# Kernel optimization log

Hardware: AMD Instinct MI355X
Metric: run time of the kernel (lower is better)

The kernel has to match this reference:

```python
import jax, jax.numpy as jnp
import numpy as np
import math

N_HEAD = 8
N_EMBD = 128  # per-head dim and input feature dim
WIN_LEN = 2048
SUB_LEN = 64
Q_LEN = 5
BATCH = 2
NEG = -1e9


def _row_mask(index, sub_len, win_len):
    log_l = math.ceil(np.log2(sub_len))
    mask = np.zeros(win_len, dtype=np.float32)
    if (win_len // sub_len) * 2 * log_l > index:
        mask[: index + 1] = 1
    else:
        while index >= 0:
            if index - log_l + 1 < 0:
                mask[:index] = 1
                break
            mask[index - log_l + 1 : index + 1] = 1  # local attention
            for i in range(log_l):
                new_index = index - log_l + 1 - 2 ** i
                if (index - new_index) <= sub_len and new_index >= 0:
                    mask[new_index] = 1  # restart attention
            index -= sub_len
    return mask


def log_mask(win_len, sub_len):
    m = np.stack([_row_mask(i, sub_len, win_len) for i in range(win_len)], axis=0)
    return m.reshape(1, 1, win_len, win_len)


def entmax15(X):
    # 1.5-entmax along the last axis, full sort (k=None path of the torch code)
    X = (X - jnp.max(X, axis=-1, keepdims=True)) * 0.5
    Xsrt = -jnp.sort(-X, axis=-1)  # descending
    d = X.shape[-1]
    rho = jnp.arange(1, d + 1, dtype=X.dtype)
    mean = jnp.cumsum(Xsrt, axis=-1) / rho
    mean_sq = jnp.cumsum(Xsrt * Xsrt, axis=-1) / rho
    ss = rho * (mean_sq - mean * mean)
    delta = (1.0 - ss) / rho
    tau = mean - jnp.sqrt(jnp.clip(delta, 0.0))
    support_size = jnp.sum(tau <= Xsrt, axis=-1, keepdims=True)
    tau_star = jnp.take_along_axis(tau, support_size - 1, axis=-1)
    Y = jnp.clip(X - tau_star, 0.0)
    return Y * Y


def setup_inputs() -> dict:
    key = jax.random.key(0)
    ks = jax.random.split(key, 5)
    H, D = N_HEAD, N_EMBD
    x = jax.random.normal(ks[0], (BATCH, WIN_LEN, D), dtype=jnp.float32)
    mask = jnp.asarray(log_mask(WIN_LEN, SUB_LEN))
    std = 0.02
    w_qk = jax.random.normal(ks[1], (2 * H * D, D, Q_LEN), dtype=jnp.float32) * std
    b_qk = jnp.zeros((2 * H * D,), jnp.float32)
    w_v = jax.random.normal(ks[2], (D, H * D), dtype=jnp.float32) * std
    b_v = jnp.zeros((H * D,), jnp.float32)
    w_proj = jax.random.normal(ks[3], (H * D, D), dtype=jnp.float32) * std
    b_proj = jnp.zeros((D,), jnp.float32)
    return {"x": x, "mask": mask, "w_qk": w_qk, "b_qk": b_qk,
            "w_v": w_v, "b_v": b_v, "w_proj": w_proj, "b_proj": b_proj}


def reference(x, mask, w_qk, b_qk, w_v, b_v, w_proj, b_proj):
    B, S, D = x.shape
    H = N_HEAD
    # value projection (Conv1D rf=1 == linear)
    value = x @ w_v + b_v                              # [B,S,H*D]
    # causal conv for query/key: left-pad by q_len-1
    xc = jnp.transpose(x, (0, 2, 1))                   # [B,D,S]
    qk = jax.lax.conv_general_dilated(
        xc, w_qk, window_strides=(1,), padding=[(Q_LEN - 1, 0)],
        dimension_numbers=("NCH", "OIH", "NCH"))       # [B,2HD,S]
    qk = jnp.transpose(qk, (0, 2, 1)) + b_qk           # [B,S,2HD]
    query, key = jnp.split(qk, 2, axis=-1)
    q = query.reshape(B, S, H, D).transpose(0, 2, 1, 3)   # [B,H,S,D]
    k = key.reshape(B, S, H, D).transpose(0, 2, 1, 3)     # [B,H,S,D]
    v = value.reshape(B, S, H, D).transpose(0, 2, 1, 3)   # [B,H,S,D]
    pre = jnp.einsum("bhqd,bhkd->bhqk", q, k)            # [B,H,S,S]
    pre = pre / jnp.sqrt(jnp.asarray(D, pre.dtype))      # scale=True
    m = mask[:, :, :S, :S]
    pre = pre * m + NEG * (1.0 - m)
    att = entmax15(pre)                                  # sparse normalizer
    # dropout is identity in eval mode
    out = jnp.einsum("bhqk,bhkd->bhqd", att, v)          # [B,H,S,D]
    out = out.transpose(0, 2, 1, 3).reshape(B, S, H * D)  # merge heads
    out = out @ w_proj + b_proj                           # c_proj
    return out
```

## Files before the change

### kernel.cpp

```cpp
#include <hip/hip_runtime.h>
#include <hip/hip_bf16.h>
#include <hip/hip_fp16.h>

#define S_LEN 2048
#define BATCH 2
#define DIM 128
#define NH 8
#define HD 1024
#define QL 5
#define KKTOT 640
#define OCH 2048
#define MAXNNZ 384

typedef _Float16 hv2 __attribute__((ext_vector_type(2)));
typedef _Float16 f16x8 __attribute__((ext_vector_type(8)));
typedef float f32x4 __attribute__((ext_vector_type(4)));

#if defined(__has_builtin)
#  if __has_builtin(__builtin_amdgcn_fdot2)
#    define USE_FDOT2 1
#  endif
#endif
#ifndef USE_FDOT2
#  define USE_FDOT2 0
#endif

__device__ __forceinline__ hv2 u2h(unsigned u) {
    union { unsigned u; hv2 h; } c; c.u = u; return c.h;
}
__device__ __forceinline__ float dot2acc(unsigned a, unsigned b, float acc) {
#if USE_FDOT2
    return __builtin_amdgcn_fdot2(u2h(a), u2h(b), acc, false);
#else
    hv2 ha = u2h(a), hb = u2h(b);
    return acc + (float)ha[0] * (float)hb[0] + (float)ha[1] * (float)hb[1];
#endif
}

__global__ void k_cvt_x(const float4* __restrict__ src, ushort4* __restrict__ dst, int n4) {
    int i = blockIdx.x * 256 + threadIdx.x;
    if (i >= n4) return;
    float4 v = src[i];
    ushort4 o;
    o.x = __half_as_ushort(__float2half(v.x));
    o.y = __half_as_ushort(__float2half(v.y));
    o.z = __half_as_ushort(__float2half(v.z));
    o.w = __half_as_ushort(__float2half(v.w));
    dst[i] = o;
}

__global__ void k_wqk_t(const float* __restrict__ w, _Float16* __restrict__ bt) {
    int j = blockIdx.x * 256 + threadIdx.x;
    if (j >= OCH * KKTOT) return;
    int o = j / KKTOT;
    int k = j % KKTOT;
    int t = k >> 7, i = k & 127;
    bt[j] = (_Float16)w[(size_t)o * KKTOT + i * QL + t];
}

__global__ void k_wv_t(const float* __restrict__ wv, _Float16* __restrict__ wvt) {
    int j = blockIdx.x * 256 + threadIdx.x;
    if (j >= HD * DIM) return;
    int c = j >> 7, k = j & 127;
    wvt[j] = (_Float16)wv[(size_t)k * HD + c];
}

__global__ void k_wp_t(const float* __restrict__ wp, _Float16* __restrict__ wpt) {
    int j = blockIdx.x * 256 + threadIdx.x;
    if (j >= DIM * HD) return;
    int c = j >> 10, k = j & 1023;
    wpt[j] = (_Float16)wp[(size_t)k * DIM + c];
}

__global__ void k_mask_csr(const float* __restrict__ mask, unsigned* __restrict__ cnt,
                           unsigned* __restrict__ idx) {
    __shared__ unsigned s_base;
    __shared__ unsigned s_wcnt[4];
    int r = blockIdx.x;
    int tid = threadIdx.x;
    int lane = tid & 63;
    int w = tid >> 6;
    if (tid == 0) s_base = 0;
    __syncthreads();
    for (int c0 = 0; c0 < S_LEN; c0 += 256) {
        int c = c0 + tid;
        bool act = mask[(size_t)r * S_LEN + c] > 0.5f;
        unsigned long long bal = __ballot(act);
        if (lane == 0) s_wcnt[w] = (unsigned)__popcll(bal);
        __syncthreads();
        unsigned off = s_base;
        for (int i = 0; i < w; i++) off += s_wcnt[i];
        off += (unsigned)__popcll(bal & ((1ull << lane) - 1ull));
        if (act && off < MAXNNZ) idx[r * MAXNNZ + off] = (unsigned)c;
        __syncthreads();
        if (tid == 0) s_base += s_wcnt[0] + s_wcnt[1] + s_wcnt[2] + s_wcnt[3];
        __syncthreads();
    }
    if (tid == 0) cnt[r] = (s_base < MAXNNZ) ? s_base : MAXNNZ;
}

template<bool CONV, int KSTEPS, int NN, typename OutT>
__global__ void __launch_bounds__(256) k_gemm16(const _Float16* __restrict__ A,
                                                const _Float16* __restrict__ Bt,
                                                const float* __restrict__ bias,
                                                OutT* __restrict__ C) {
    const int K = KSTEPS * 32;
    int tid = threadIdx.x;
    int lane = tid & 63, wave = tid >> 6;
    int wr = wave >> 1, wc = wave & 1;
    int l15 = lane & 15, lk = lane >> 4;
    int rbase = blockIdx.x * 64;
    int batch = rbase >> 11;
    int s0 = rbase & 2047;
    f32x4 acc[2][2] = {};
    for (int ks = 0; ks < KSTEPS; ks++) {
        int t = CONV ? (ks >> 2) : 0;
        int i0 = CONV ? ((ks & 3) * 32) : (ks * 32);
        f16x8 afr[2], bfr[2];
#pragma unroll
        for (int a = 0; a < 2; a++) {
            int srow = s0 + wr * 32 + a * 16 + l15;
            int sx = CONV ? (srow - (QL - 1) + t) : srow;
            int sclamp = sx < 0 ? 0 : sx;
            f16x8 av = *reinterpret_cast<const f16x8*>(
                A + ((size_t)(batch * S_LEN + sclamp)) * (CONV ? DIM : (K)) + i0 + lk * 8);
            if (CONV && sx < 0) av = f16x8{0, 0, 0, 0, 0, 0, 0, 0};
            afr[a] = av;
        }
#pragma unroll
        for (int bb = 0; bb < 2; bb++) {
            int col = blockIdx.y * 64 + wc * 32 + bb * 16 + l15;
            bfr[bb] = *reinterpret_cast<const f16x8*>(Bt + (size_t)col * K + ks * 32 + lk * 8);
        }
#pragma unroll
        for (int a = 0; a < 2; a++)
#pragma unroll
            for (int bb = 0; bb < 2; bb++)
                acc[a][bb] = __builtin_amdgcn_mfma_f32_16x16x32_f16(afr[a], bfr[bb], acc[a][bb], 0, 0, 0);
    }
#pragma unroll
    for (int a = 0; a < 2; a++)
#pragma unroll
        for (int bb = 0; bb < 2; bb++) {
            int col = blockIdx.y * 64 + wc * 32 + bb * 16 + l15;
            float bs = bias[col];
#pragma unroll
            for (int j = 0; j < 4; j++) {
                int row = rbase + wr * 32 + a * 16 + lk * 4 + j;
                C[(size_t)row * NN + col] = (OutT)(acc[a][bb][j] + bs);
            }
        }
}

__global__ void __launch_bounds__(256) k_attn(const _Float16* __restrict__ qk16,
                                              const _Float16* __restrict__ val16,
                                              const unsigned* __restrict__ cnt,
                                              const unsigned* __restrict__ idxbuf,
                                              _Float16* __restrict__ attout) {
    __shared__ float ssc[MAXNNZ];
    __shared__ unsigned sidx[MAXNNZ];
    __shared__ float pvs[16][128];
    int l = blockIdx.x;
    int bid = (l & 7) * 4096 + (l >> 3);
    int r = bid & (S_LEN - 1);
    int h = (bid >> 11) & (NH - 1);
    int b = bid >> 14;
    int tid = threadIdx.x;
    int lane = tid & 63;
    int wave = tid >> 6;
    int n = (int)cnt[r];
    const float scale = 0.08838834764831843f;

    for (int j = tid; j < n; j += 256) sidx[j] = idxbuf[r * MAXNNZ + j];
    __syncthreads();

    {
        int grp = tid >> 2;
        int ll  = tid & 3;
        const uint4* q16 = reinterpret_cast<const uint4*>(
                               qk16 + ((size_t)(b * S_LEN + r)) * OCH + h * 128);
        uint4 qreg[4];
#pragma unroll
        for (int i = 0; i < 4; i++) qreg[i] = q16[i * 4 + ll];
        const _Float16* kbase = qk16 + (size_t)b * S_LEN * OCH + HD + h * 128;
        for (int j = grp; j < n; j += 64) {
            const uint4* kp = reinterpret_cast<const uint4*>(kbase + (size_t)sidx[j] * OCH);
            float p = 0.f;
#pragma unroll
            for (int i = 0; i < 4; i++) {
                uint4 kv = kp[i * 4 + ll];
                const unsigned* ka = reinterpret_cast<const unsigned*>(&kv);
                const unsigned* qa = reinterpret_cast<const unsigned*>(&qreg[i]);
                p = dot2acc(qa[0], ka[0], p);
                p = dot2acc(qa[1], ka[1], p);
                p = dot2acc(qa[2], ka[2], p);
                p = dot2acc(qa[3], ka[3], p);
            }
            p += __shfl_xor(p, 1, 64);
            p += __shfl_xor(p, 2, 64);
            if (ll == 0) ssc[j] = p * scale;
        }
    }
    __syncthreads();

    if (wave == 0) {
        float xl[6];
        float mx = -3.0e38f;
#pragma unroll
        for (int l2 = 0; l2 < 6; l2++) {
            int j = lane + 64 * l2;
            xl[l2] = (j < n) ? ssc[j] * 0.5f : -3.0e38f;
            mx = fmaxf(mx, xl[l2]);
        }
#pragma unroll
        for (int off = 32; off >= 1; off >>= 1) mx = fmaxf(mx, __shfl_xor(mx, off, 64));
        float tau = mx - 1.f;
        for (int it = 0; it < 12; it++) {
            float s1 = 0.f, s2 = 0.f;
#pragma unroll
            for (int l2 = 0; l2 < 6; l2++) {
                float d = fmaxf(xl[l2] - tau, 0.f);
                s1 += d;
                s2 += d * d;
            }
#pragma unroll
            for (int off = 32; off >= 1; off >>= 1) {
                s1 += __shfl_xor(s1, off, 64);
                s2 += __shfl_xor(s2, off, 64);
            }
            tau += (s2 - 1.f) / (2.f * s1);
        }
#pragma unroll
        for (int l2 = 0; l2 < 6; l2++) {
            int j = lane + 64 * l2;
            if (j < n) {
                float d = fmaxf(xl[l2] - tau, 0.f);
                ssc[j] = d * d;
            }
        }
    }
    __syncthreads();

    {
        int slot = tid >> 4;
        int dg   = tid & 15;
        const uint4* vbase = reinterpret_cast<const uint4*>(
                                 val16 + (size_t)b * S_LEN * HD + h * 128) + dg;
        float acc[8];
#pragma unroll
        for (int k = 0; k < 8; k++) acc[k] = 0.f;
        for (int j = slot; j < n; j += 16) {
            float w = ssc[j];
            uint4 vv = vbase[(size_t)sidx[j] << 7];
            const __half2* va = reinterpret_cast<const __half2*>(&vv);
#pragma unroll
            for (int k = 0; k < 4; k++) {
                float2 f = __half22float2(va[k]);
                acc[2 * k]     += w * f.x;
                acc[2 * k + 1] += w * f.y;
            }
        }
#pragma unroll
        for (int k = 0; k < 8; k++) pvs[slot][dg * 8 + k] = acc[k];
    }
    __syncthreads();
    if (tid < 128) {
        float a = 0.f;
#pragma unroll
        for (int s = 0; s < 16; s++) a += pvs[s][tid];
        attout[((size_t)(b * S_LEN + r)) * HD + h * 128 + tid] = (_Float16)a;
    }
}

extern "C" void kernel_launch(void* const* d_in, const int* in_sizes, int n_in,
                              void* d_out, int out_size, void* d_ws, size_t ws_size,
                              hipStream_t stream) {
    const float* x      = (const float*)d_in[0];
    const float* mask   = (const float*)d_in[1];
    const float* w_qk   = (const float*)d_in[2];
    const float* b_qk   = (const float*)d_in[3];
    const float* w_v    = (const float*)d_in[4];
    const float* b_v    = (const float*)d_in[5];
    const float* w_proj = (const float*)d_in[6];
    const float* b_proj = (const float*)d_in[7];
    float* out = (float*)d_out;

    char* ws = (char*)d_ws;
    _Float16*  x16   = (_Float16*)(ws + 0);
    _Float16*  qk16  = (_Float16*)(ws + 1048576);
    _Float16*  val16 = (_Float16*)(ws + 17825792);
    _Float16*  bt16  = (_Float16*)(ws + 26214400);
    _Float16*  wvt   = (_Float16*)(ws + 28835840);
    _Float16*  wpt   = (_Float16*)(ws + 29097984);
    unsigned*  cnt   = (unsigned*)(ws + 29360128);
    unsigned*  idx   = (unsigned*)(ws + 29368320);
    _Float16*  ao16  = (_Float16*)(ws + 32514048);

    hipLaunchKernelGGL(k_cvt_x, dim3(BATCH * S_LEN * DIM / 4 / 256), dim3(256), 0, stream,
                       (const float4*)x, (ushort4*)x16, BATCH * S_LEN * DIM / 4);
    hipLaunchKernelGGL(k_wqk_t, dim3(OCH * KKTOT / 256), dim3(256), 0, stream, w_qk, bt16);
    hipLaunchKernelGGL(k_wv_t, dim3(HD * DIM / 256), dim3(256), 0, stream, w_v, wvt);
    hipLaunchKernelGGL(k_wp_t, dim3(DIM * HD / 256), dim3(256), 0, stream, w_proj, wpt);
    hipLaunchKernelGGL(k_mask_csr, dim3(S_LEN), dim3(256), 0, stream, mask, cnt, idx);
    hipLaunchKernelGGL((k_gemm16<false, 4, HD, _Float16>), dim3(BATCH * S_LEN / 64, HD / 64), dim3(256), 0, stream,
                       x16, wvt, b_v, val16);
    hipLaunchKernelGGL((k_gemm16<true, 20, OCH, _Float16>), dim3(BATCH * S_LEN / 64, OCH / 64), dim3(256), 0, stream,
                       x16, bt16, b_qk, qk16);
    hipLaunchKernelGGL(k_attn, dim3(BATCH * NH * S_LEN), dim3(256), 0, stream, qk16, val16, cnt, idx, ao16);
    hipLaunchKernelGGL((k_gemm16<false, 32, DIM, float>), dim3(BATCH * S_LEN / 64, DIM / 64), dim3(256), 0, stream,
                       ao16, wpt, b_proj, out);
}
```

Before: 325.1 us.

## Fuse prep conversion kernels, pad PV smem, vectorize stores, cut entmax iterations

Merges the four conversion and transpose kernels into one launch covering all ranges, which removes three kernel launches. It also pads the shared partial-sum array to avoid bank conflicts, writes the partials with float4 stores, and runs two fewer Newton iterations for the entmax threshold. Fewer iterations trade some accuracy of tau for less work. The x conversion is now scalar rather than float4, which may cost some bandwidth.

Result: faster. 309.1 us (-4.9%).

```diff
diff --git a/kernel.cpp b/kernel.cpp
--- a/kernel.cpp
+++ b/kernel.cpp
@@ -37,39 +37,33 @@
 #endif
 }
 
-__global__ void k_cvt_x(const float4* __restrict__ src, ushort4* __restrict__ dst, int n4) {
+__global__ void k_prep(const float* __restrict__ x, const float* __restrict__ w_qk,
+                       const float* __restrict__ wv, const float* __restrict__ wp,
+                       _Float16* __restrict__ x16, _Float16* __restrict__ bt,
+                       _Float16* __restrict__ wvt, _Float16* __restrict__ wpt) {
     int i = blockIdx.x * 256 + threadIdx.x;
-    if (i >= n4) return;
-    float4 v = src[i];
-    ushort4 o;
-    o.x = __half_as_ushort(__float2half(v.x));
-    o.y = __half_as_ushort(__float2half(v.y));
-    o.z = __half_as_ushort(__float2half(v.z));
-    o.w = __half_as_ushort(__float2half(v.w));
-    dst[i] = o;
-}
-
-__global__ void k_wqk_t(const float* __restrict__ w, _Float16* __restrict__ bt) {
-    int j = blockIdx.x * 256 + threadIdx.x;
-    if (j >= OCH * KKTOT) return;
-    int o = j / KKTOT;
-    int k = j % KKTOT;
-    int t = k >> 7, i = k & 127;
-    bt[j] = (_Float16)w[(size_t)o * KKTOT + i * QL + t];
-}
-
-__global__ void k_wv_t(const float* __restrict__ wv, _Float16* __restrict__ wvt) {
-    int j = blockIdx.x * 256 + threadIdx.x;
-    if (j >= HD * DIM) return;
-    int c = j >> 7, k = j & 127;
-    wvt[j] = (_Float16)wv[(size_t)k * HD + c];
-}
-
-__global__ void k_wp_t(const float* __restrict__ wp, _Float16* __restrict__ wpt) {
-    int j = blockIdx.x * 256 + threadIdx.x;
-    if (j >= DIM * HD) return;
-    int c = j >> 10, k = j & 1023;
-    wpt[j] = (_Float16)wp[(size_t)k * DIM + c];
+    if (i < OCH * KKTOT) {
+        int o = i / KKTOT, k = i % KKTOT;
+        int t = k >> 7, ii = k & 127;
+        bt[i] = (_Float16)w_qk[(size_t)o * KKTOT + ii * QL + t];
+        return;
+    }
+    i -= OCH * KKTOT;
+    if (i < BATCH * S_LEN * DIM) {
+        x16[i] = (_Float16)x[i];
+        return;
+    }
+    i -= BATCH * S_LEN * DIM;
+    if (i < HD * DIM) {
+        int c = i >> 7, k = i & 127;
+        wvt[i] = (_Float16)wv[(size_t)k * HD + c];
+        return;
+    }
+    i -= HD * DIM;
+    if (i < DIM * HD) {
+        int c = i >> 10, k = i & 1023;
+        wpt[i] = (_Float16)wp[(size_t)k * DIM + c];
+    }
 }
 
 __global__ void k_mask_csr(const float* __restrict__ mask, unsigned* __restrict__ cnt,
@@ -159,7 +153,7 @@
                                               _Float16* __restrict__ attout) {
     __shared__ float ssc[MAXNNZ];
     __shared__ unsigned sidx[MAXNNZ];
-    __shared__ float pvs[16][128];
+    __shared__ float pvs[16][136];
     int l = blockIdx.x;
     int bid = (l & 7) * 4096 + (l >> 3);
     int r = bid & (S_LEN - 1);
@@ -215,7 +209,7 @@
 #pragma unroll
         for (int off = 32; off >= 1; off >>= 1) mx = fmaxf(mx, __shfl_xor(mx, off, 64));
         float tau = mx - 1.f;
-        for (int it = 0; it < 12; it++) {
+        for (int it = 0; it < 10; it++) {
             float s1 = 0.f, s2 = 0.f;
 #pragma unroll
             for (int l2 = 0; l2 < 6; l2++) {
@@ -260,8 +254,10 @@
                 acc[2 * k + 1] += w * f.y;
             }
         }
-#pragma unroll
-        for (int k = 0; k < 8; k++) pvs[slot][dg * 8 + k] = acc[k];
+        float4 v0 = {acc[0], acc[1], acc[2], acc[3]};
+        float4 v1 = {acc[4], acc[5], acc[6], acc[7]};
+        *reinterpret_cast<float4*>(&pvs[slot][dg * 8]) = v0;
+        *reinterpret_cast<float4*>(&pvs[slot][dg * 8 + 4]) = v1;
     }
     __syncthreads();
     if (tid < 128) {
@@ -296,11 +292,8 @@
     unsigned*  idx   = (unsigned*)(ws + 29368320);
     _Float16*  ao16  = (_Float16*)(ws + 32514048);
 
-    hipLaunchKernelGGL(k_cvt_x, dim3(BATCH * S_LEN * DIM / 4 / 256), dim3(256), 0, stream,
-                       (const float4*)x, (ushort4*)x16, BATCH * S_LEN * DIM / 4);
-    hipLaunchKernelGGL(k_wqk_t, dim3(OCH * KKTOT / 256), dim3(256), 0, stream, w_qk, bt16);
-    hipLaunchKernelGGL(k_wv_t, dim3(HD * DIM / 256), dim3(256), 0, stream, w_v, wvt);
-    hipLaunchKernelGGL(k_wp_t, dim3(DIM * HD / 256), dim3(256), 0, stream, w_proj, wpt);
+    hipLaunchKernelGGL(k_prep, dim3(8192), dim3(256), 0, stream,
+                       x, w_qk, w_v, w_proj, x16, bt16, wvt, wpt);
     hipLaunchKernelGGL(k_mask_csr, dim3(S_LEN), dim3(256), 0, stream, mask, cnt, idx);
     hipLaunchKernelGGL((k_gemm16<false, 4, HD, _Float16>), dim3(BATCH * S_LEN / 64, HD / 64), dim3(256), 0, stream,
                        x16, wvt, b_v, val16);
```
